# Kernel optimization log

Hardware: AMD Instinct MI355X
Metric: run time of the kernel (lower is better)

Reference implementation:

```python
import jax, jax.numpy as jnp
import numpy as np

B, T, D, TY = 64, 512, 96, 512
H, DK = 4, 32            # num_heads, embed_dim_per_head
E = H * DK               # embed_dim = 128
P = 2                    # function='L' -> 2 coefficients
L, HID = 64, 128         # latent_dim, hidden_dim


def setup_inputs() -> dict:
    key = jax.random.key(0)
    ks = jax.random.split(key, 16)
    inp = {
        "timesteps": jax.random.uniform(ks[0], (B, T), jnp.float32),
        "X": jax.random.normal(ks[1], (B, T, D), jnp.float32),
        "M": jax.random.randint(ks[2], (B, T, D), 0, 2).astype(jnp.float32),
        "y_time_steps": jax.random.uniform(ks[3], (B, TY), jnp.float32),
        # time_embedding: Linear(1, E)
        "te_w": jax.random.normal(ks[4], (E,), jnp.float32),
        "te_b": jax.random.normal(ks[5], (E,), jnp.float32) * 0.1,
        # learned query [1, P, E]
        "query": jax.random.normal(ks[6], (1, P, E), jnp.float32),
        # query_map / key_map: Linear(E, E), stored [in, out]
        "q_w": jax.random.normal(ks[7], (E, E), jnp.float32) / np.sqrt(E),
        "q_b": jax.random.normal(ks[8], (E,), jnp.float32) * 0.1,
        "k_w": jax.random.normal(ks[9], (E, E), jnp.float32) / np.sqrt(E),
        "k_b": jax.random.normal(ks[10], (E,), jnp.float32) * 0.1,
        # attn shared out: Linear(2D*H, L)
        "ow": jax.random.normal(ks[11], (2 * D * H, L), jnp.float32) / np.sqrt(2 * D * H),
        "ob": jnp.zeros((L,), jnp.float32),
        # decoder MLP: Linear(L,HID)+ReLU+Linear(HID,D)
        "w1": jax.random.normal(ks[12], (L, HID), jnp.float32) / np.sqrt(L),
        "b1": jnp.zeros((HID,), jnp.float32),
        "w2": jax.random.normal(ks[13], (HID, D), jnp.float32) / np.sqrt(HID),
        "b2": jnp.zeros((D,), jnp.float32),
    }
    return inp


def _fld_forward(timesteps, X, M, y_time_steps, te_w, te_b, query,
                 q_w, q_b, k_w, k_b, ow, ob, w1, b1, w2, b2):
    b, t, d = X.shape
    # time embedding: Linear(1,E), sin applied to indices i % H == 0
    emb = timesteps[..., None] * te_w + te_b               # [B,T,E]
    sin_idx = (jnp.arange(E) % H) == 0
    emb = jnp.where(sin_idx, jnp.sin(emb), emb)

    X_cat = jnp.concatenate([X, M], axis=-1)               # [B,T,2D]
    M_cat = jnp.concatenate([M, M], axis=-1)               # [B,T,2D]

    q = query @ q_w + q_b                                   # [1,P,E]
    k = emb @ k_w + k_b                                     # [B,T,E]
    q = q.reshape(1, P, H, DK).transpose(0, 2, 1, 3)        # [1,H,P,dk]
    k = k.reshape(b, t, H, DK).transpose(0, 2, 1, 3)        # [B,H,T,dk]

    scores = jnp.einsum('xhpd,bhtd->bhpt', q, k) / np.sqrt(DK)  # [B,H,P,T]
    # broadcast over value feature dim, mask per-feature, softmax over T
    logits = jnp.where(M_cat[:, None, None, :, :] == 0, -jnp.inf,
                       scores[..., None])                   # [B,H,P,T,2D]
    p = jax.nn.softmax(logits, axis=-2)
    xa = jnp.einsum('bhptf,btf->bhpf', p, X_cat)            # [B,H,P,2D]
    xa = xa.transpose(0, 2, 1, 3).reshape(b, P, H * 2 * d)  # [B,P,H*2D]
    coeffs = xa @ ow + ob                                   # [B,P,L]

    # function 'L': linear in y_time_steps
    x = coeffs[:, 0][:, None, :] + y_time_steps[:, :, None] * coeffs[:, 1][:, None, :]
    h1 = jax.nn.relu(x @ w1 + b1)
    return h1 @ w2 + b2                                     # [B,TY,D]


def reference(timesteps, X, M, y_time_steps, te_w, te_b, query,
              q_w, q_b, k_w, k_b, ow, ob, w1, b1, w2, b2):
    return _fld_forward(timesteps, X, M, y_time_steps, te_w, te_b, query,
                        q_w, q_b, k_w, k_b, ow, ob, w1, b1, w2, b2)
```

## Files before the change

### kernel.cpp

```cpp
#include <hip/hip_runtime.h>
#include <math.h>

#define B_   64
#define T_   512
#define D_   96
#define TY_  512
#define H_   4
#define DK_  32
#define E_   128
#define P_   2
#define L_   64
#define HID_ 128

#define WS_PN    2048
#define WS_PD    395264
#define WS_AB    788480

__global__ __launch_bounds__(256) void kspool(
    const float* __restrict__ tsteps, const float* __restrict__ te_w,
    const float* __restrict__ te_b,   const float* __restrict__ X,
    const float* __restrict__ M,      const float* __restrict__ query,
    const float* __restrict__ q_w,    const float* __restrict__ q_b,
    const float* __restrict__ k_w,    const float* __restrict__ k_b,
    float* __restrict__ ws)
{
    const int c = blockIdx.x, b = blockIdx.y, tid = threadIdx.x;
    __shared__ float qm[P_ * E_];
    __shared__ float w2q_s[E_ * 8];
    __shared__ float tw_s[E_], tb_s[E_], bq_s[8];
    __shared__ float w_s[64 * 8];
    __shared__ float red[96 * 17];

    {
        int p = tid >> 7, ep = tid & 127;
        float acc = q_b[ep];
        #pragma unroll 4
        for (int e = 0; e < E_; ++e)
            acc += query[p * E_ + e] * q_w[e * E_ + ep];
        qm[p * E_ + ep] = acc;
    }
    if (tid < E_) { tw_s[tid] = te_w[tid]; tb_s[tid] = te_b[tid]; }
    __syncthreads();
    const float rs = 0.17677669529663687f;
    #pragma unroll
    for (int i = 0; i < 4; ++i) {
        int idx = tid + i * 256;
        int e = idx >> 3, hp = idx & 7, h = hp >> 1, p = hp & 1;
        float acc = 0.f;
        #pragma unroll
        for (int dk = 0; dk < DK_; ++dk)
            acc += k_w[e * E_ + h * DK_ + dk] * qm[p * E_ + h * DK_ + dk];
        w2q_s[idx] = acc * rs;
    }
    if (tid < 8) {
        int hp = tid, h = hp >> 1, p = hp & 1;
        float acc = 0.f;
        #pragma unroll
        for (int dk = 0; dk < DK_; ++dk)
            acc += k_b[h * DK_ + dk] * qm[p * E_ + h * DK_ + dk];
        bq_s[hp] = acc * rs;
    }
    __syncthreads();

    {
        const int t = tid & 63, hpg = tid >> 6, hp0 = hpg * 2;
        const float tv = tsteps[b * T_ + c * 64 + t];
        float a0 = 0.f, a1 = 0.f;
        #pragma unroll 4
        for (int e = 0; e < E_; ++e) {
            float v = tv * tw_s[e] + tb_s[e];
            if ((e & 3) == 0) v = __sinf(v);
            float2 w = *(const float2*)&w2q_s[e * 8 + hp0];
            a0 += v * w.x;
            a1 += v * w.y;
        }
        w_s[t * 8 + hp0]     = __expf(a0 + bq_s[hp0]);
        w_s[t * 8 + hp0 + 1] = __expf(a1 + bq_s[hp0 + 1]);
    }
    __syncthreads();

    const int fid = tid & 127, slice = tid >> 7;
    float num[8] = {0.f, 0.f, 0.f, 0.f, 0.f, 0.f, 0.f, 0.f};
    float den[8] = {0.f, 0.f, 0.f, 0.f, 0.f, 0.f, 0.f, 0.f};
    if (fid < 96) {
        #pragma unroll 4
        for (int i = 0; i < 32; ++i) {
            int tl = slice + 2 * i;
            size_t base = ((size_t)(b * T_ + c * 64 + tl)) * D_ + fid;
            float m = M[base], x = X[base];
            float mx = m * x;
            const float* wr = w_s + tl * 8;
            #pragma unroll
            for (int hp = 0; hp < 8; ++hp) {
                num[hp] += wr[hp] * mx;
                den[hp] += wr[hp] * m;
            }
        }
    }
    __syncthreads();
    if (slice == 1 && fid < 96) {
        #pragma unroll
        for (int hp = 0; hp < 8; ++hp) {
            red[fid * 17 + hp]     = num[hp];
            red[fid * 17 + 8 + hp] = den[hp];
        }
    }
    __syncthreads();
    if (slice == 0 && fid < 96) {
        float* pN = ws + WS_PN + ((size_t)((b * 8 + c) * 8)) * 96;
        float* pD = ws + WS_PD + ((size_t)((b * 8 + c) * 8)) * 96;
        #pragma unroll
        for (int hp = 0; hp < 8; ++hp) {
            pN[hp * 96 + fid] = num[hp] + red[fid * 17 + hp];
            pD[hp * 96 + fid] = den[hp] + red[fid * 17 + 8 + hp];
        }
    }
}

__global__ __launch_bounds__(512) void kcoef(
    const float* __restrict__ ow, const float* __restrict__ w1,
    const float* __restrict__ b1, const float* __restrict__ ob,
    float* __restrict__ ws)
{
    const int b = blockIdx.x, tid = threadIdx.x;
    __shared__ float xa_s[8 * 96];
    __shared__ float obp[8][64];
    __shared__ float cfp[4][2][64];
    __shared__ float cf_s[2][64];
    __shared__ float abp[4][2][128];

    for (int flat = tid; flat < 8 * 96; flat += 512) {
        int hp = flat / 96, f = flat - hp * 96;
        float n = 0.f, d = 0.f;
        #pragma unroll
        for (int c = 0; c < 8; ++c) {
            n += ws[WS_PN + ((size_t)((b * 8 + c) * 8 + hp)) * 96 + f];
            d += ws[WS_PD + ((size_t)((b * 8 + c) * 8 + hp)) * 96 + f];
        }
        xa_s[flat] = n / d;
    }
    {
        int g = tid >> 6, l = tid & 63;
        float acc = 0.f;
        #pragma unroll 4
        for (int k = 0; k < 48; ++k) {
            int hj = g * 48 + k, h = hj / 96, j = hj - h * 96;
            acc += ow[(size_t)(h * 2 * D_ + D_ + j) * L_ + l];
        }
        obp[g][l] = acc;
    }
    __syncthreads();

    {
        int h = tid >> 7, p = (tid >> 6) & 1, l = tid & 63;
        const float* xr = xa_s + (h * 2 + p) * 96;
        const float* owr = ow + (size_t)(h * 2 * D_) * L_ + l;
        float acc = 0.f;
        #pragma unroll 4
        for (int f = 0; f < 96; ++f)
            acc += xr[f] * owr[(size_t)f * L_];
        cfp[h][p][l] = acc;
    }
    __syncthreads();

    if (tid < 128) {
        int p = tid >> 6, l = tid & 63;
        float v = cfp[0][p][l] + cfp[1][p][l] + cfp[2][p][l] + cfp[3][p][l] + ob[l];
        #pragma unroll
        for (int g = 0; g < 8; ++g) v += obp[g][l];
        cf_s[p][l] = v;
    }
    __syncthreads();

    {
        int s = tid >> 7, j = tid & 127;
        float a0 = 0.f, a1 = 0.f;
        #pragma unroll
        for (int li = 0; li < 16; ++li) {
            int l = s * 16 + li;
            float wv = w1[l * HID_ + j];
            a0 += cf_s[0][l] * wv;
            a1 += cf_s[1][l] * wv;
        }
        abp[s][0][j] = a0;
        abp[s][1][j] = a1;
    }
    __syncthreads();

    if (tid < 256) {
        int q = tid >> 7, j = tid & 127;
        float v = abp[0][q][j] + abp[1][q][j] + abp[2][q][j] + abp[3][q][j];
        if (q == 0) v += b1[j];
        ws[WS_AB + b * 256 + q * 128 + j] = v;
    }
}

__global__ __launch_bounds__(256) void kdec(
    const float* __restrict__ yts, const float* __restrict__ w2,
    const float* __restrict__ b2,  const float* __restrict__ ws,
    float* __restrict__ out)
{
    __shared__ float h_s[HID_ * 64];
    __shared__ float y_s[64];
    __shared__ float a0_s[HID_], a1_s[HID_];
    const int tid = threadIdx.x;
    const int posb = blockIdx.x * 64;
    const int b = posb >> 9;

    if (tid < 64) y_s[tid] = yts[posb + tid];
    if (tid >= 64 && tid < 192) {
        int j = tid - 64;
        a0_s[j] = ws[WS_AB + b * 256 + j];
        a1_s[j] = ws[WS_AB + b * 256 + 128 + j];
    }
    __syncthreads();

    #pragma unroll 4
    for (int r = 0; r < 32; ++r) {
        int flat = r * 256 + tid;
        int j = flat >> 6, pos = flat & 63;
        h_s[flat] = fmaxf(0.f, a0_s[j] + y_s[pos] * a1_s[j]);
    }
    __syncthreads();

    const int pg = tid >> 4, dg = tid & 15;
    const int p0 = pg * 4, d0 = dg * 6;
    float acc[4][6];
    #pragma unroll
    for (int pp = 0; pp < 4; ++pp)
        #pragma unroll
        for (int dd = 0; dd < 6; ++dd) acc[pp][dd] = 0.f;

    #pragma unroll 2
    for (int j = 0; j < HID_; ++j) {
        float4 h4 = *(const float4*)&h_s[j * 64 + p0];
        const float* wr = w2 + j * D_ + d0;
        float wv[6];
        #pragma unroll
        for (int dd = 0; dd < 6; ++dd) wv[dd] = wr[dd];
        const float hv[4] = {h4.x, h4.y, h4.z, h4.w};
        #pragma unroll
        for (int pp = 0; pp < 4; ++pp)
            #pragma unroll
            for (int dd = 0; dd < 6; ++dd)
                acc[pp][dd] += hv[pp] * wv[dd];
    }

    float bv[6];
    #pragma unroll
    for (int dd = 0; dd < 6; ++dd) bv[dd] = b2[d0 + dd];
    #pragma unroll
    for (int pp = 0; pp < 4; ++pp) {
        size_t ob = ((size_t)(posb + p0 + pp)) * D_ + d0;
        #pragma unroll
        for (int dd = 0; dd < 6; ++dd) out[ob + dd] = acc[pp][dd] + bv[dd];
    }
}

extern "C" void kernel_launch(void* const* d_in, const int* in_sizes, int n_in,
                              void* d_out, int out_size, void* d_ws, size_t ws_size,
                              hipStream_t stream)
{
    const float* timesteps = (const float*)d_in[0];
    const float* X         = (const float*)d_in[1];
    const float* M         = (const float*)d_in[2];
    const float* yts       = (const float*)d_in[3];
    const float* te_w      = (const float*)d_in[4];
    const float* te_b      = (const float*)d_in[5];
    const float* query     = (const float*)d_in[6];
    const float* q_w       = (const float*)d_in[7];
    const float* q_b       = (const float*)d_in[8];
    const float* k_w       = (const float*)d_in[9];
    const float* k_b       = (const float*)d_in[10];
    const float* ow        = (const float*)d_in[11];
    const float* ob        = (const float*)d_in[12];
    const float* w1        = (const float*)d_in[13];
    const float* b1        = (const float*)d_in[14];
    const float* w2        = (const float*)d_in[15];
    const float* b2        = (const float*)d_in[16];
    float* out = (float*)d_out;
    float* ws  = (float*)d_ws;

    kspool<<<dim3(8, B_), 256, 0, stream>>>(timesteps, te_w, te_b, X, M,
                                            query, q_w, q_b, k_w, k_b, ws);
    kcoef<<<B_, 512, 0, stream>>>(ow, w1, b1, ob, ws);
    kdec<<<(B_ * TY_) / 64, 256, 0, stream>>>(yts, w2, b2, ws, out);
}
```

Baseline: 165.4 us.

## Fuse coefficient computation into decoder kernel and move ow column-sum into kspool

Removes the separate per-batch coefficient kernel. Each of the 512 decoder blocks now recomputes its batch's attention-pooled coefficients and the first-layer affine terms from the partial num/den workspace. The ow mask-half column sum, which does not depend on the input, is computed once by the batch-0 blocks of kspool and stored in the workspace. This saves a launch and a dependency stage, but the coefficient work is repeated 8 times per batch, adding redundant ow and w1 reads.

```diff
diff --git a/kernel.cpp b/kernel.cpp
--- a/kernel.cpp
+++ b/kernel.cpp
@@ -12,9 +12,9 @@
 #define L_   64
 #define HID_ 128
 
+#define WS_OB2P  1024
 #define WS_PN    2048
 #define WS_PD    395264
-#define WS_AB    788480
 
 __global__ __launch_bounds__(256) void kspool(
     const float* __restrict__ tsteps, const float* __restrict__ te_w,
@@ -22,7 +22,7 @@
     const float* __restrict__ M,      const float* __restrict__ query,
     const float* __restrict__ q_w,    const float* __restrict__ q_b,
     const float* __restrict__ k_w,    const float* __restrict__ k_b,
-    float* __restrict__ ws)
+    const float* __restrict__ ow,     float* __restrict__ ws)
 {
     const int c = blockIdx.x, b = blockIdx.y, tid = threadIdx.x;
     __shared__ float qm[P_ * E_];
@@ -30,6 +30,7 @@
     __shared__ float tw_s[E_], tb_s[E_], bq_s[8];
     __shared__ float w_s[64 * 8];
     __shared__ float red[96 * 17];
+    __shared__ float obp2[4][64];
 
     {
         int p = tid >> 7, ep = tid & 127;
@@ -115,21 +116,45 @@
             pD[hp * 96 + fid] = den[hp] + red[fid * 17 + 8 + hp];
         }
     }
+
+    if (b == 0) {
+        int sub = tid >> 6, l = tid & 63;
+        float acc = 0.f;
+        #pragma unroll
+        for (int k = 0; k < 12; ++k) {
+            int hj = c * 48 + sub * 12 + k;
+            int h = hj / 96, j = hj - h * 96;
+            acc += ow[(size_t)(h * 2 * D_ + D_ + j) * L_ + l];
+        }
+        obp2[sub][l] = acc;
+        __syncthreads();
+        if (sub == 0)
+            ws[WS_OB2P + c * 64 + l] = obp2[0][l] + obp2[1][l] + obp2[2][l] + obp2[3][l];
+    }
 }
 
-__global__ __launch_bounds__(512) void kcoef(
-    const float* __restrict__ ow, const float* __restrict__ w1,
-    const float* __restrict__ b1, const float* __restrict__ ob,
-    float* __restrict__ ws)
+__global__ __launch_bounds__(256) void kdecf(
+    const float* __restrict__ yts, const float* __restrict__ ow,
+    const float* __restrict__ w1,  const float* __restrict__ b1,
+    const float* __restrict__ ob,  const float* __restrict__ w2,
+    const float* __restrict__ b2,  const float* __restrict__ ws,
+    float* __restrict__ out)
 {
-    const int b = blockIdx.x, tid = threadIdx.x;
     __shared__ float xa_s[8 * 96];
-    __shared__ float obp[8][64];
     __shared__ float cfp[4][2][64];
     __shared__ float cf_s[2][64];
-    __shared__ float abp[4][2][128];
-
-    for (int flat = tid; flat < 8 * 96; flat += 512) {
+    __shared__ float abp[2][2][128];
+    __shared__ float a0_s[HID_], a1_s[HID_];
+    __shared__ float y_s[64];
+    __shared__ float h_s[HID_ * 64];
+    const int tid = threadIdx.x;
+    const int bx = blockIdx.x;
+    const int b = bx >> 3;
+    const int posb = bx * 64;
+
+    if (tid < 64) y_s[tid] = yts[posb + tid];
+
+    for (int flat = tid; flat < 8 * 96; flat += 256) {
         int hp = flat / 96, f = flat - hp * 96;
         float n = 0.f, d = 0.f;
         #pragma unroll
@@ -139,20 +164,12 @@
         }
         xa_s[flat] = n / d;
     }
-    {
-        int g = tid >> 6, l = tid & 63;
-        float acc = 0.f;
-        #pragma unroll 4
-        for (int k = 0; k < 48; ++k) {
-            int hj = g * 48 + k, h = hj / 96, j = hj - h * 96;
-            acc += ow[(size_t)(h * 2 * D_ + D_ + j) * L_ + l];
-        }
-        obp[g][l] = acc;
-    }
-    __syncthreads();
-
-    {
-        int h = tid >> 7, p = (tid >> 6) & 1, l = tid & 63;
+    __syncthreads();
+
+    #pragma unroll
+    for (int it = 0; it < 2; ++it) {
+        int idx = tid + it * 256;
+        int h = idx >> 7, p = (idx >> 6) & 1, l = idx & 63;
         const float* xr = xa_s + (h * 2 + p) * 96;
         const float* owr = ow + (size_t)(h * 2 * D_) * L_ + l;
         float acc = 0.f;
@@ -167,7 +184,7 @@
         int p = tid >> 6, l = tid & 63;
         float v = cfp[0][p][l] + cfp[1][p][l] + cfp[2][p][l] + cfp[3][p][l] + ob[l];
         #pragma unroll
-        for (int g = 0; g < 8; ++g) v += obp[g][l];
+        for (int g = 0; g < 8; ++g) v += ws[WS_OB2P + g * 64 + l];
         cf_s[p][l] = v;
     }
     __syncthreads();
@@ -175,9 +192,9 @@
     {
         int s = tid >> 7, j = tid & 127;
         float a0 = 0.f, a1 = 0.f;
-        #pragma unroll
-        for (int li = 0; li < 16; ++li) {
-            int l = s * 16 + li;
+        #pragma unroll 4
+        for (int li = 0; li < 32; ++li) {
+            int l = s * 32 + li;
             float wv = w1[l * HID_ + j];
             a0 += cf_s[0][l] * wv;
             a1 += cf_s[1][l] * wv;
@@ -187,31 +204,11 @@
     }
     __syncthreads();
 
-    if (tid < 256) {
-        int q = tid >> 7, j = tid & 127;
-        float v = abp[0][q][j] + abp[1][q][j] + abp[2][q][j] + abp[3][q][j];
-        if (q == 0) v += b1[j];
-        ws[WS_AB + b * 256 + q * 128 + j] = v;
-    }
-}
-
-__global__ __launch_bounds__(256) void kdec(
-    const float* __restrict__ yts, const float* __restrict__ w2,
-    const float* __restrict__ b2,  const float* __restrict__ ws,
-    float* __restrict__ out)
-{
-    __shared__ float h_s[HID_ * 64];
-    __shared__ float y_s[64];
-    __shared__ float a0_s[HID_], a1_s[HID_];
-    const int tid = threadIdx.x;
-    const int posb = blockIdx.x * 64;
-    const int b = posb >> 9;
-
-    if (tid < 64) y_s[tid] = yts[posb + tid];
-    if (tid >= 64 && tid < 192) {
-        int j = tid - 64;
-        a0_s[j] = ws[WS_AB + b * 256 + j];
-        a1_s[j] = ws[WS_AB + b * 256 + 128 + j];
+    if (tid < 128) {
+        a0_s[tid] = abp[0][0][tid] + abp[1][0][tid] + b1[tid];
+    } else {
+        int j = tid - 128;
+        a1_s[j] = abp[0][1][j] + abp[1][1][j];
     }
     __syncthreads();
 
@@ -251,9 +248,9 @@
     for (int dd = 0; dd < 6; ++dd) bv[dd] = b2[d0 + dd];
     #pragma unroll
     for (int pp = 0; pp < 4; ++pp) {
-        size_t ob = ((size_t)(posb + p0 + pp)) * D_ + d0;
-        #pragma unroll
-        for (int dd = 0; dd < 6; ++dd) out[ob + dd] = acc[pp][dd] + bv[dd];
+        size_t obase = ((size_t)(posb + p0 + pp)) * D_ + d0;
+        #pragma unroll
+        for (int dd = 0; dd < 6; ++dd) out[obase + dd] = acc[pp][dd] + bv[dd];
     }
 }
 
@@ -282,7 +279,6 @@
     float* ws  = (float*)d_ws;
 
     kspool<<<dim3(8, B_), 256, 0, stream>>>(timesteps, te_w, te_b, X, M,
-                                            query, q_w, q_b, k_w, k_b, ws);
-    kcoef<<<B_, 512, 0, stream>>>(ow, w1, b1, ob, ws);
-    kdec<<<(B_ * TY_) / 64, 256, 0, stream>>>(yts, w2, b2, ws, out);
+                                            query, q_w, q_b, k_w, k_b, ow, ws);
+    kdecf<<<(B_ * TY_) / 64, 256, 0, stream>>>(yts, ow, w1, b1, ob, w2, b2, ws, out);
 }
```

Result: no change. 168.5 us (+1.9%).
